# Performance work log

Measured on AMD Instinct MI355X. Metric: run time of the kernel, lower is better.

The kernel has to match this reference:

```python
import jax, jax.numpy as jnp
import numpy as np

B, T, D_IN, D_OUT, N_HEAD = 4, 2048, 1024, 1024, 16
HEAD_DIM = D_OUT // N_HEAD


def setup_inputs() -> dict:
    key = jax.random.key(0)
    ks = jax.random.split(key, 6)
    s_in = 1.0 / np.sqrt(D_IN)
    s_out = 1.0 / np.sqrt(D_OUT)
    return {
        "x": jax.random.normal(ks[0], (B, T, D_IN), dtype=jnp.float32),
        "Wq": jax.random.uniform(ks[1], (D_OUT, D_IN), jnp.float32, -s_in, s_in),
        "Wk": jax.random.uniform(ks[2], (D_OUT, D_IN), jnp.float32, -s_in, s_in),
        "Wv": jax.random.uniform(ks[3], (D_OUT, D_IN), jnp.float32, -s_in, s_in),
        "Wo": jax.random.uniform(ks[4], (D_OUT, D_OUT), jnp.float32, -s_out, s_out),
        "bo": jax.random.uniform(ks[5], (D_OUT,), jnp.float32, -s_out, s_out),
    }


def reference(x, Wq, Wk, Wv, Wo, bo):
    Bx, Tx, _ = x.shape
    # torch Linear: y = x @ W.T
    def heads(W):
        h = jnp.einsum("btc,dc->btd", x, W)
        return h.reshape(Bx, Tx, N_HEAD, HEAD_DIM).transpose(0, 2, 1, 3)  # [B,H,T,hd]
    q, k, v = heads(Wq), heads(Wk), heads(Wv)
    scores = jnp.einsum("bhqd,bhkd->bhqk", q, k)  # [B,H,T,T]
    causal = jnp.triu(jnp.ones((Tx, Tx), dtype=bool), k=1)
    scores = jnp.where(causal, -jnp.inf, scores)
    att = jax.nn.softmax(scores / np.sqrt(HEAD_DIM), axis=-1)
    ctx = jnp.einsum("bhqk,bhkd->bhqd", att, v)
    ctx = ctx.transpose(0, 2, 1, 3).reshape(Bx, Tx, D_OUT)
    return jnp.einsum("btd,od->bto", ctx, Wo) + bo
```

## Files before the change

### kernel.cpp

```cpp
#include <hip/hip_runtime.h>
#include <math.h>

typedef __attribute__((ext_vector_type(8))) short vbf8;
typedef __attribute__((ext_vector_type(4))) short vbf4;
typedef __attribute__((ext_vector_type(4))) float vf4;
typedef __attribute__((ext_vector_type(2))) unsigned int vu2;

__device__ __forceinline__ short f2bf(float f) {
  union { float f; unsigned int u; } v; v.f = f;
  unsigned int r = v.u + 0x7fffu + ((v.u >> 16) & 1u);
  return (short)(r >> 16);
}
__device__ __forceinline__ unsigned int cvtpk(float a, float b) {
  unsigned int r;
  asm("v_cvt_pk_bf16_f32 %0, %1, %2" : "=v"(r) : "v"(a), "v"(b));
  return r;
}
__device__ __forceinline__ float fexp2(float x) {
#if __has_builtin(__builtin_amdgcn_exp2f)
  return __builtin_amdgcn_exp2f(x);
#else
  return exp2f(x);
#endif
}

__device__ __forceinline__ void gload16(const void* g, void* l) {
  __builtin_amdgcn_global_load_lds(
      (const __attribute__((address_space(1))) unsigned int*)g,
      (__attribute__((address_space(3))) unsigned int*)l, 16, 0, 0);
}

__global__ __launch_bounds__(256) void cvt_kernel(const float* __restrict__ src,
                                                  short* __restrict__ dst, int n) {
  int i = (blockIdx.x * 256 + threadIdx.x) * 4;
  if (i >= n) return;
  float4 v = *(const float4*)(src + i);
  vu2 o;
  o.x = cvtpk(v.x, v.y);
  o.y = cvtpk(v.z, v.w);
  *(vu2*)(dst + i) = o;
}

__global__ __launch_bounds__(256) void cvtw_kernel(
    const float* __restrict__ Wq, const float* __restrict__ Wk,
    const float* __restrict__ Wv, short* __restrict__ wqkv) {
  const int bid = blockIdx.x;
  const int wsel = bid >> 10;
  const int off = ((bid & 1023) * 256 + threadIdx.x) * 4;
  const float* s = (wsel == 0) ? Wq : (wsel == 1) ? Wk : Wv;
  float4 v = *(const float4*)(s + off);
  vu2 o;
  o.x = cvtpk(v.x, v.y);
  o.y = cvtpk(v.z, v.w);
  *(vu2*)(wqkv + wsel * 1048576 + off) = o;
}

template <int EPI>
__global__ __launch_bounds__(256) void gemm_bt(
    const short* __restrict__ A, const short* __restrict__ Bw, int K,
    short* __restrict__ qb, short* __restrict__ kb, short* __restrict__ vtb,
    const float* __restrict__ bo, float* __restrict__ outp) {
  __shared__ __align__(16) short As[128 * 32];
  __shared__ __align__(16) short Bs[128 * 32];
  const int lane = threadIdx.x & 63;
  const int w = threadIdx.x >> 6;
  const int wr = w >> 1, wc = w & 1;

  const unsigned flat = blockIdx.y * gridDim.x + blockIdx.x;
  const unsigned cpx = (gridDim.x * gridDim.y) >> 3;
  const unsigned swz = (flat & 7) * cpx + (flat >> 3);
  const int m0 = (int)(swz / gridDim.x) * 128, n0 = (int)(swz % gridDim.x) * 128;

  const short* ga = A + (size_t)(m0 + w * 32 + (lane >> 2)) * K + (lane & 3) * 8;
  const short* gb = Bw + (size_t)(n0 + w * 32 + (lane >> 2)) * K + (lane & 3) * 8;
  short* lA = As + w * 1024;
  short* lB = Bs + w * 1024;

  vf4 acc[4][4];
#pragma unroll
  for (int i = 0; i < 4; ++i)
#pragma unroll
    for (int j = 0; j < 4; ++j) acc[i][j] = (vf4){0.f, 0.f, 0.f, 0.f};

  const int ar = wr * 64 + (lane & 15);
  const int br = wc * 64 + (lane & 15);
  const int kk = (lane >> 4) * 8;

  for (int k0 = 0; k0 < K; k0 += 32) {
    gload16(ga + k0, lA);
    gload16(ga + k0 + 16 * K, lA + 512);
    gload16(gb + k0, lB);
    gload16(gb + k0 + 16 * K, lB + 512);
    __syncthreads();
    vbf8 af[4], bfr[4];
#pragma unroll
    for (int mf = 0; mf < 4; ++mf) af[mf] = *(const vbf8*)(As + (ar + mf * 16) * 32 + kk);
#pragma unroll
    for (int nf = 0; nf < 4; ++nf) bfr[nf] = *(const vbf8*)(Bs + (br + nf * 16) * 32 + kk);
#pragma unroll
    for (int mf = 0; mf < 4; ++mf)
#pragma unroll
      for (int nf = 0; nf < 4; ++nf)
        acc[mf][nf] = __builtin_amdgcn_mfma_f32_16x16x32_bf16(af[mf], bfr[nf], acc[mf][nf], 0, 0, 0);
    __syncthreads();
  }

#pragma unroll
  for (int mf = 0; mf < 4; ++mf) {
    const int mbase = m0 + wr * 64 + mf * 16 + (lane >> 4) * 4;
#pragma unroll
    for (int nf = 0; nf < 4; ++nf) {
      vf4 v = acc[mf][nf];
      const int n = n0 + wc * 64 + nf * 16 + (lane & 15);
      if (EPI == 0) {
        const int region = n >> 10;
        const int nn = n & 1023;
        const int h = nn >> 6, d = nn & 63;
        if (region == 0) {
#pragma unroll
          for (int i = 0; i < 4; ++i) {
            const int m = mbase + i;
            const int b = m >> 11, t = m & 2047;
            qb[((size_t)(b * 16 + h) * 2048 + t) * 64 + d] = f2bf(v[i] * 0.1803368801111204f);
          }
        } else if (region == 1) {
#pragma unroll
          for (int i = 0; i < 4; ++i) {
            const int m = mbase + i;
            const int b = m >> 11, t = m & 2047;
            kb[((size_t)(b * 16 + h) * 2048 + t) * 64 + d] = f2bf(v[i]);
          }
        } else {
          const int b = mbase >> 11, t = mbase & 2047;
          vbf4 o;
          o.x = f2bf(v.x); o.y = f2bf(v.y); o.z = f2bf(v.z); o.w = f2bf(v.w);
          *(vbf4*)(vtb + ((size_t)(b * 16 + h) * 64 + d) * 2048 + t) = o;
        }
      } else {
        const float bias = bo[n];
#pragma unroll
        for (int i = 0; i < 4; ++i) {
          const int m = mbase + i;
          outp[(size_t)m * 1024 + n] = v[i] + bias;
        }
      }
    }
  }
}

__global__ __launch_bounds__(64) void attn_kernel(
    const short* __restrict__ Qh, const short* __restrict__ Kh,
    const short* __restrict__ Vt, short* __restrict__ ctx) {
  __shared__ __align__(16) short Ps[16 * 68];

  const int lane = threadIdx.x;
  const int l15 = lane & 15, g = lane >> 4;
  const int bid = blockIdx.x;
  const int x = bid & 7;
  const int kidx = bid >> 3;
  const int p_idx = kidx & 7;
  const int W = 31 - (kidx >> 3);
  const int pair = x + 8 * p_idx;
  const int b = pair >> 4, h = pair & 15;

  const size_t bhoff = (size_t)pair * 131072;
  const short* Qp = Qh + bhoff;
  const short* Kp = Kh + bhoff;
  const short* Vp = Vt + bhoff;
  const int wq0 = W * 64;

  vbf8 qfr[4][2];
#pragma unroll
  for (int qfi = 0; qfi < 4; ++qfi)
#pragma unroll
    for (int ks = 0; ks < 2; ++ks)
      qfr[qfi][ks] = *(const vbf8*)(Qp + (size_t)(wq0 + qfi * 16 + l15) * 64 +
                                    ks * 32 + g * 8);

  vf4 o2[4][4];
  float mrow[4], lrow[4];
#pragma unroll
  for (int qfi = 0; qfi < 4; ++qfi) {
#pragma unroll
    for (int df = 0; df < 4; ++df) o2[qfi][df] = (vf4){0.f, 0.f, 0.f, 0.f};
    mrow[qfi] = -1e30f; lrow[qfi] = 0.f;
  }

  const int nt = W + 1;

  vbf8 kA[4][2], kB[4][2];
  auto loadK = [&](int tt, vbf8 (&kd)[4][2]) {
    const int kb0 = tt * 64;
#pragma unroll
    for (int kf = 0; kf < 4; ++kf)
#pragma unroll
      for (int ks = 0; ks < 2; ++ks)
        kd[kf][ks] = *(const vbf8*)(Kp + (size_t)(kb0 + kf * 16 + l15) * 64 +
                                    ks * 32 + g * 8);
  };
  loadK(0, kA);

  auto tile = [&](int t, vbf8 (&kc)[4][2], vbf8 (&kn)[4][2]) {
    const int k0 = t * 64;

    vbf8 vb[2][4];
#pragma unroll
    for (int ks2 = 0; ks2 < 2; ++ks2)
#pragma unroll
      for (int df = 0; df < 4; ++df)
        vb[ks2][df] = *(const vbf8*)(Vp + (size_t)(df * 16 + l15) * 2048 +
                                     k0 + ks2 * 32 + g * 8);
    if (t + 1 < nt) loadK(t + 1, kn);

#pragma unroll
    for (int qfi = 0; qfi < 4; ++qfi) {
      const int q = wq0 + qfi * 16 + l15;
      const bool needmask = (k0 + 64 > wq0 + qfi * 16);

      vf4 s[4];
      __builtin_amdgcn_s_setprio(1);
#pragma unroll
      for (int kf = 0; kf < 4; ++kf) {
        s[kf] = (vf4){0.f, 0.f, 0.f, 0.f};
#pragma unroll
        for (int ks = 0; ks < 2; ++ks)
          s[kf] = __builtin_amdgcn_mfma_f32_16x16x32_bf16(kc[kf][ks], qfr[qfi][ks],
                                                          s[kf], 0, 0, 0);
      }
      __builtin_amdgcn_s_setprio(0);

      if (needmask) {
#pragma unroll
        for (int kf = 0; kf < 4; ++kf) {
          const int kbase = k0 + kf * 16 + g * 4;
#pragma unroll
          for (int i = 0; i < 4; ++i)
            if (kbase + i > q) s[kf][i] = -1e30f;
        }
      }
      float t0 = fmaxf(fmaxf(s[0][0], s[0][1]), fmaxf(s[0][2], s[0][3]));
      float t1 = fmaxf(fmaxf(s[1][0], s[1][1]), fmaxf(s[1][2], s[1][3]));
      float t2 = fmaxf(fmaxf(s[2][0], s[2][1]), fmaxf(s[2][2], s[2][3]));
      float t3 = fmaxf(fmaxf(s[3][0], s[3][1]), fmaxf(s[3][2], s[3][3]));
      const float mxl = fmaxf(fmaxf(t0, t1), fmaxf(t2, t3));

      float mn = mrow[qfi];
      if (!__all((int)(mxl - mn <= 8.f))) {
        float mx = fmaxf(mxl, __shfl_xor(mxl, 16));
        mx = fmaxf(mx, __shfl_xor(mx, 32));
        mn = fmaxf(mrow[qfi], mx);
        const float al = fexp2(mrow[qfi] - mn);
        mrow[qfi] = mn;
        lrow[qfi] *= al;
#pragma unroll
        for (int df = 0; df < 4; ++df)
#pragma unroll
          for (int i = 0; i < 4; ++i) o2[qfi][df][i] *= al;
      }

      float rs = 0.f;
#pragma unroll
      for (int kf = 0; kf < 4; ++kf)
#pragma unroll
        for (int i = 0; i < 4; ++i) {
          const float p = fexp2(s[kf][i] - mn);
          s[kf][i] = p;
          rs += p;
        }
      lrow[qfi] += rs;

#pragma unroll
      for (int kf = 0; kf < 4; ++kf) {
        vu2 pk;
        pk.x = cvtpk(s[kf][0], s[kf][1]);
        pk.y = cvtpk(s[kf][2], s[kf][3]);
        *(vu2*)(Ps + l15 * 68 + kf * 16 + g * 4) = pk;
      }

      vbf8 pb[2];
#pragma unroll
      for (int ks2 = 0; ks2 < 2; ++ks2)
        pb[ks2] = *(const vbf8*)(Ps + l15 * 68 + ks2 * 32 + g * 8);

      __builtin_amdgcn_s_setprio(1);
#pragma unroll
      for (int ks2 = 0; ks2 < 2; ++ks2)
#pragma unroll
        for (int df = 0; df < 4; ++df)
          o2[qfi][df] = __builtin_amdgcn_mfma_f32_16x16x32_bf16(vb[ks2][df], pb[ks2],
                                                                o2[qfi][df], 0, 0, 0);
      __builtin_amdgcn_s_setprio(0);
    }
  };

  for (int t = 0; t < nt; t += 2) {
    tile(t, kA, kB);
    if (t + 1 < nt) tile(t + 1, kB, kA);
  }

#pragma unroll
  for (int qfi = 0; qfi < 4; ++qfi) {
    float lsum = lrow[qfi];
    lsum += __shfl_xor(lsum, 16);
    lsum += __shfl_xor(lsum, 32);
    const float inv = 1.f / lsum;
    const int q = wq0 + qfi * 16 + l15;
    short* dst = ctx + (size_t)(b * 2048 + q) * 1024 + h * 64;
#pragma unroll
    for (int df = 0; df < 4; ++df) {
      vu2 o;
      o.x = cvtpk(o2[qfi][df][0] * inv, o2[qfi][df][1] * inv);
      o.y = cvtpk(o2[qfi][df][2] * inv, o2[qfi][df][3] * inv);
      *(vu2*)(dst + df * 16 + g * 4) = o;
    }
  }
}

extern "C" void kernel_launch(void* const* d_in, const int* in_sizes, int n_in,
                              void* d_out, int out_size, void* d_ws, size_t ws_size,
                              hipStream_t stream) {
  const float* x  = (const float*)d_in[0];
  const float* Wq = (const float*)d_in[1];
  const float* Wk = (const float*)d_in[2];
  const float* Wv = (const float*)d_in[3];
  const float* Wo = (const float*)d_in[4];
  const float* bo = (const float*)d_in[5];
  float* out = (float*)d_out;

  char* ws = (char*)d_ws;
  short* xb   = (short*)(ws);
  short* wqkv = (short*)(ws + 16777216);
  short* qb   = (short*)(ws + 23068672);
  short* kb   = (short*)(ws + 39845888);
  short* vtb  = (short*)(ws + 56623104);
  short* ctxb = xb;
  short* wob  = wqkv;

  cvt_kernel<<<8192, 256, 0, stream>>>(x, xb, 8388608);
  cvtw_kernel<<<3072, 256, 0, stream>>>(Wq, Wk, Wv, wqkv);
  gemm_bt<0><<<dim3(24, 64), 256, 0, stream>>>(xb, wqkv, 1024, qb, kb, vtb, nullptr, nullptr);
  cvt_kernel<<<1024, 256, 0, stream>>>(Wo, wob, 1048576);
  attn_kernel<<<2048, 64, 0, stream>>>(qb, kb, vtb, ctxb);
  gemm_bt<1><<<dim3(8, 64), 256, 0, stream>>>(ctxb, wob, 1024, nullptr, nullptr, nullptr, bo, out);
}
```

Before: 206.9 us.

## Replace QKV projection GEMM with 256x256-tile double-buffered kernel using direct global-to-LDS loads

The QKV projection GEMM now uses a new 512-thread kernel with 256x256 output tiles and a K-step of 64. It double-buffers LDS with gload16 direct global-to-shared loads, XOR-swizzles the LDS layout, and sets explicit waitcnt, barrier and priority scheduling. The goal is more data reuse per tile and hiding global load latency behind MFMA work. The cost is a large LDS footprint (128KB) and only 384 blocks, which may leave CUs idle and limit occupancy. The output projection keeps the old 128x128 kernel, now specialized without the template.

```diff
diff --git a/kernel.cpp b/kernel.cpp
--- a/kernel.cpp
+++ b/kernel.cpp
@@ -55,10 +55,125 @@
   *(vu2*)(wqkv + wsel * 1048576 + off) = o;
 }
 
-template <int EPI>
-__global__ __launch_bounds__(256) void gemm_bt(
+__global__ __launch_bounds__(512) void gemm256(
+    const short* __restrict__ A, const short* __restrict__ Bw,
+    short* __restrict__ qb, short* __restrict__ kb, short* __restrict__ vtb) {
+  __shared__ __align__(16) short As[2][16384];
+  __shared__ __align__(16) short Bs[2][16384];
+  const int tid = threadIdx.x;
+  const int lane = tid & 63;
+  const int w = tid >> 6;
+  const int wr = w >> 2, wc = w & 3;
+  const int l15 = lane & 15, g = lane >> 4;
+  const int K = 1024;
+
+  const unsigned flat = blockIdx.y * gridDim.x + blockIdx.x;
+  const unsigned cpx = (gridDim.x * gridDim.y) >> 3;
+  const unsigned swz = (flat & 7) * cpx + (flat >> 3);
+  const int m0 = (int)(swz / gridDim.x) * 256;
+  const int n0 = (int)(swz % gridDim.x) * 256;
+
+  const int srow = w * 32 + (lane >> 3);
+  const int scol = ((lane & 7) ^ (lane >> 3)) * 8;
+  const short* gA = A + (size_t)(m0 + srow) * K + scol;
+  const short* gB = Bw + (size_t)(n0 + srow) * K + scol;
+
+  vf4 acc[8][4];
+#pragma unroll
+  for (int i = 0; i < 8; ++i)
+#pragma unroll
+    for (int j = 0; j < 4; ++j) acc[i][j] = (vf4){0.f, 0.f, 0.f, 0.f};
+
+  auto stage2 = [&](int t, int bb, int q) {
+    const int koff = t * 64;
+    gload16(gA + (size_t)q * 8 * K + koff, &As[bb][(w * 32 + q * 8) * 64]);
+    gload16(gB + (size_t)q * 8 * K + koff, &Bs[bb][(w * 32 + q * 8) * 64]);
+  };
+
+#pragma unroll
+  for (int q = 0; q < 4; ++q) stage2(0, 0, q);
+
+  const int NT = 16;
+  for (int t = 0; t < NT; ++t) {
+    const int bb = t & 1;
+    vbf8 bfr[4][2];
+#pragma unroll
+    for (int q = 0; q < 4; ++q) {
+      if (t + 1 < NT) stage2(t + 1, bb ^ 1, q);
+      if (q == 0) {
+        if (t + 1 < NT) asm volatile("s_waitcnt vmcnt(2)" ::: "memory");
+        else            asm volatile("s_waitcnt vmcnt(0)" ::: "memory");
+        __builtin_amdgcn_s_barrier();
+#pragma unroll
+        for (int nf = 0; nf < 4; ++nf)
+#pragma unroll
+          for (int ks = 0; ks < 2; ++ks) {
+            const int r = wc * 64 + nf * 16 + l15;
+            const int c = (ks * 32 + g * 8) ^ ((r & 7) * 8);
+            bfr[nf][ks] = *(const vbf8*)(&Bs[bb][r * 64 + c]);
+          }
+      }
+      vbf8 afr[2][2];
+#pragma unroll
+      for (int i = 0; i < 2; ++i)
+#pragma unroll
+        for (int ks = 0; ks < 2; ++ks) {
+          const int r = wr * 128 + (q * 2 + i) * 16 + l15;
+          const int c = (ks * 32 + g * 8) ^ ((r & 7) * 8);
+          afr[i][ks] = *(const vbf8*)(&As[bb][r * 64 + c]);
+        }
+      asm volatile("s_waitcnt lgkmcnt(0)" ::: "memory");
+      __builtin_amdgcn_sched_barrier(0);
+      __builtin_amdgcn_s_setprio(1);
+#pragma unroll
+      for (int i = 0; i < 2; ++i)
+#pragma unroll
+        for (int nf = 0; nf < 4; ++nf)
+#pragma unroll
+          for (int ks = 0; ks < 2; ++ks)
+            acc[q * 2 + i][nf] = __builtin_amdgcn_mfma_f32_16x16x32_bf16(
+                afr[i][ks], bfr[nf][ks], acc[q * 2 + i][nf], 0, 0, 0);
+      __builtin_amdgcn_s_setprio(0);
+      if (q == 3) __builtin_amdgcn_s_barrier();
+    }
+  }
+
+#pragma unroll
+  for (int mf = 0; mf < 8; ++mf) {
+    const int mbase = m0 + wr * 128 + mf * 16 + g * 4;
+#pragma unroll
+    for (int nf = 0; nf < 4; ++nf) {
+      vf4 v = acc[mf][nf];
+      const int n = n0 + wc * 64 + nf * 16 + l15;
+      const int region = n >> 10;
+      const int nn = n & 1023;
+      const int h = nn >> 6, d = nn & 63;
+      if (region == 0) {
+#pragma unroll
+        for (int i = 0; i < 4; ++i) {
+          const int m = mbase + i;
+          const int b = m >> 11, tt = m & 2047;
+          qb[((size_t)(b * 16 + h) * 2048 + tt) * 64 + d] = f2bf(v[i] * 0.1803368801111204f);
+        }
+      } else if (region == 1) {
+#pragma unroll
+        for (int i = 0; i < 4; ++i) {
+          const int m = mbase + i;
+          const int b = m >> 11, tt = m & 2047;
+          kb[((size_t)(b * 16 + h) * 2048 + tt) * 64 + d] = f2bf(v[i]);
+        }
+      } else {
+        const int b = mbase >> 11, tt = mbase & 2047;
+        vbf4 o;
+        o.x = f2bf(v.x); o.y = f2bf(v.y); o.z = f2bf(v.z); o.w = f2bf(v.w);
+        *(vbf4*)(vtb + ((size_t)(b * 16 + h) * 64 + d) * 2048 + tt) = o;
+      }
+    }
+  }
+}
+
+__global__ __launch_bounds__(256) void gemm_bt1(
     const short* __restrict__ A, const short* __restrict__ Bw, int K,
-    short* __restrict__ qb, short* __restrict__ kb, short* __restrict__ vtb,
     const float* __restrict__ bo, float* __restrict__ outp) {
   __shared__ __align__(16) short As[128 * 32];
   __shared__ __align__(16) short Bs[128 * 32];
@@ -112,37 +227,11 @@
     for (int nf = 0; nf < 4; ++nf) {
       vf4 v = acc[mf][nf];
       const int n = n0 + wc * 64 + nf * 16 + (lane & 15);
-      if (EPI == 0) {
-        const int region = n >> 10;
-        const int nn = n & 1023;
-        const int h = nn >> 6, d = nn & 63;
-        if (region == 0) {
-#pragma unroll
-          for (int i = 0; i < 4; ++i) {
-            const int m = mbase + i;
-            const int b = m >> 11, t = m & 2047;
-            qb[((size_t)(b * 16 + h) * 2048 + t) * 64 + d] = f2bf(v[i] * 0.1803368801111204f);
-          }
-        } else if (region == 1) {
-#pragma unroll
-          for (int i = 0; i < 4; ++i) {
-            const int m = mbase + i;
-            const int b = m >> 11, t = m & 2047;
-            kb[((size_t)(b * 16 + h) * 2048 + t) * 64 + d] = f2bf(v[i]);
-          }
-        } else {
-          const int b = mbase >> 11, t = mbase & 2047;
-          vbf4 o;
-          o.x = f2bf(v.x); o.y = f2bf(v.y); o.z = f2bf(v.z); o.w = f2bf(v.w);
-          *(vbf4*)(vtb + ((size_t)(b * 16 + h) * 64 + d) * 2048 + t) = o;
-        }
-      } else {
-        const float bias = bo[n];
-#pragma unroll
-        for (int i = 0; i < 4; ++i) {
-          const int m = mbase + i;
-          outp[(size_t)m * 1024 + n] = v[i] + bias;
-        }
+      const float bias = bo[n];
+#pragma unroll
+      for (int i = 0; i < 4; ++i) {
+        const int m = mbase + i;
+        outp[(size_t)m * 1024 + n] = v[i] + bias;
       }
     }
   }
@@ -338,8 +427,8 @@
 
   cvt_kernel<<<8192, 256, 0, stream>>>(x, xb, 8388608);
   cvtw_kernel<<<3072, 256, 0, stream>>>(Wq, Wk, Wv, wqkv);
-  gemm_bt<0><<<dim3(24, 64), 256, 0, stream>>>(xb, wqkv, 1024, qb, kb, vtb, nullptr, nullptr);
+  gemm256<<<dim3(12, 32), 512, 0, stream>>>(xb, wqkv, qb, kb, vtb);
   cvt_kernel<<<1024, 256, 0, stream>>>(Wo, wob, 1048576);
   attn_kernel<<<2048, 64, 0, stream>>>(qb, kb, vtb, ctxb);
-  gemm_bt<1><<<dim3(8, 64), 256, 0, stream>>>(ctxb, wob, 1024, nullptr, nullptr, nullptr, bo, out);
-}
+  gemm_bt1<<<dim3(8, 64), 256, 0, stream>>>(ctxb, wob, 1024, bo, out);
+}
```

New measurement: 216.4 us. 4.6% more time.

## Share K/V tiles in LDS across two waves and pair causal strips

Applied to the files above, without the earlier changes.

The attention kernel now runs two waves per block that share swizzled, double-buffered K and V tiles staged into LDS via direct global-to-LDS loads, instead of each single-wave block loading K/V into registers. Each block processes two 128-row query strips, one long and one short (15-Sp and Sp), so every block gets an equal causal workload, and the grid shrinks from 2048 to 512 blocks. The goal is to halve global K/V traffic per query row and balance causal work across blocks. In exchange it adds block-wide barriers and vmcnt waits every tile and lowers the block count. The wave owning the lower rows also idles on the final diagonal tile.

```diff
diff --git a/kernel.cpp b/kernel.cpp
--- a/kernel.cpp
+++ b/kernel.cpp
@@ -148,18 +148,22 @@
   }
 }
 
-__global__ __launch_bounds__(64) void attn_kernel(
+__global__ __launch_bounds__(128) void attn_kernel(
     const short* __restrict__ Qh, const short* __restrict__ Kh,
     const short* __restrict__ Vt, short* __restrict__ ctx) {
-  __shared__ __align__(16) short Ps[16 * 68];
-
-  const int lane = threadIdx.x;
+  __shared__ __align__(16) short Ks[2][64 * 64];
+  __shared__ __align__(16) short Vs[2][64 * 64];
+  __shared__ __align__(16) short Ps[2][16 * 68];
+
+  const int tid = threadIdx.x;
+  const int lane = tid & 63;
+  const int w = tid >> 6;
   const int l15 = lane & 15, g = lane >> 4;
   const int bid = blockIdx.x;
   const int x = bid & 7;
   const int kidx = bid >> 3;
   const int p_idx = kidx & 7;
-  const int W = 31 - (kidx >> 3);
+  const int Sp = kidx >> 3;
   const int pair = x + 8 * p_idx;
   const int b = pair >> 4, h = pair & 15;
 
@@ -167,153 +171,164 @@
   const short* Qp = Qh + bhoff;
   const short* Kp = Kh + bhoff;
   const short* Vp = Vt + bhoff;
-  const int wq0 = W * 64;
-
-  vbf8 qfr[4][2];
-#pragma unroll
-  for (int qfi = 0; qfi < 4; ++qfi)
-#pragma unroll
-    for (int ks = 0; ks < 2; ++ks)
-      qfr[qfi][ks] = *(const vbf8*)(Qp + (size_t)(wq0 + qfi * 16 + l15) * 64 +
-                                    ks * 32 + g * 8);
-
-  vf4 o2[4][4];
-  float mrow[4], lrow[4];
-#pragma unroll
-  for (int qfi = 0; qfi < 4; ++qfi) {
-#pragma unroll
-    for (int df = 0; df < 4; ++df) o2[qfi][df] = (vf4){0.f, 0.f, 0.f, 0.f};
-    mrow[qfi] = -1e30f; lrow[qfi] = 0.f;
-  }
-
-  const int nt = W + 1;
-
-  vbf8 kA[4][2], kB[4][2];
-  auto loadK = [&](int tt, vbf8 (&kd)[4][2]) {
-    const int kb0 = tt * 64;
-#pragma unroll
-    for (int kf = 0; kf < 4; ++kf)
+  const int sr = lane >> 3;
+  const int scol = ((lane & 7) ^ sr) * 8;
+  short* Pw = Ps[w];
+
+  auto runStrip = [&](int S) {
+    const int wq0 = S * 128 + w * 64;
+    const int nt = 2 * S + 2;
+
+    vbf8 qfr[4][2];
+#pragma unroll
+    for (int qfi = 0; qfi < 4; ++qfi)
 #pragma unroll
       for (int ks = 0; ks < 2; ++ks)
-        kd[kf][ks] = *(const vbf8*)(Kp + (size_t)(kb0 + kf * 16 + l15) * 64 +
-                                    ks * 32 + g * 8);
-  };
-  loadK(0, kA);
-
-  auto tile = [&](int t, vbf8 (&kc)[4][2], vbf8 (&kn)[4][2]) {
-    const int k0 = t * 64;
-
-    vbf8 vb[2][4];
-#pragma unroll
-    for (int ks2 = 0; ks2 < 2; ++ks2)
-#pragma unroll
-      for (int df = 0; df < 4; ++df)
-        vb[ks2][df] = *(const vbf8*)(Vp + (size_t)(df * 16 + l15) * 2048 +
-                                     k0 + ks2 * 32 + g * 8);
-    if (t + 1 < nt) loadK(t + 1, kn);
-
+        qfr[qfi][ks] = *(const vbf8*)(Qp + (size_t)(wq0 + qfi * 16 + l15) * 64 +
+                                      ks * 32 + g * 8);
+
+    vf4 o2[4][4];
+    float mrow[4], lrow[4];
 #pragma unroll
     for (int qfi = 0; qfi < 4; ++qfi) {
-      const int q = wq0 + qfi * 16 + l15;
-      const bool needmask = (k0 + 64 > wq0 + qfi * 16);
-
-      vf4 s[4];
-      __builtin_amdgcn_s_setprio(1);
-#pragma unroll
-      for (int kf = 0; kf < 4; ++kf) {
-        s[kf] = (vf4){0.f, 0.f, 0.f, 0.f};
-#pragma unroll
-        for (int ks = 0; ks < 2; ++ks)
-          s[kf] = __builtin_amdgcn_mfma_f32_16x16x32_bf16(kc[kf][ks], qfr[qfi][ks],
-                                                          s[kf], 0, 0, 0);
-      }
-      __builtin_amdgcn_s_setprio(0);
-
-      if (needmask) {
-#pragma unroll
-        for (int kf = 0; kf < 4; ++kf) {
-          const int kbase = k0 + kf * 16 + g * 4;
-#pragma unroll
-          for (int i = 0; i < 4; ++i)
-            if (kbase + i > q) s[kf][i] = -1e30f;
+#pragma unroll
+      for (int df = 0; df < 4; ++df) o2[qfi][df] = (vf4){0.f, 0.f, 0.f, 0.f};
+      mrow[qfi] = -1e30f; lrow[qfi] = 0.f;
+    }
+
+    auto stage = [&](int tt, int bb) {
+      const int k0s = tt * 64;
+#pragma unroll
+      for (int j = 0; j < 4; ++j)
+        gload16(Kp + (size_t)(k0s + w * 32 + j * 8 + sr) * 64 + scol,
+                &Ks[bb][(w * 32 + j * 8) * 64]);
+#pragma unroll
+      for (int j = 0; j < 4; ++j)
+        gload16(Vp + (size_t)(w * 32 + j * 8 + sr) * 2048 + k0s + scol,
+                &Vs[bb][(w * 32 + j * 8) * 64]);
+    };
+
+    stage(0, 0);
+    asm volatile("s_waitcnt vmcnt(0)" ::: "memory");
+    __builtin_amdgcn_s_barrier();
+
+    for (int t = 0; t < nt; ++t) {
+      const int bb = t & 1;
+      if (t + 1 < nt) stage(t + 1, bb ^ 1);
+
+      if (t <= 2 * S + w) {
+        const int k0 = t * 64;
+#pragma unroll
+        for (int qfi = 0; qfi < 4; ++qfi) {
+          const int q = wq0 + qfi * 16 + l15;
+          const bool needmask = (k0 + 64 > wq0 + qfi * 16);
+
+          vf4 s[4];
+          __builtin_amdgcn_s_setprio(1);
+#pragma unroll
+          for (int kf = 0; kf < 4; ++kf) {
+            s[kf] = (vf4){0.f, 0.f, 0.f, 0.f};
+#pragma unroll
+            for (int ks = 0; ks < 2; ++ks) {
+              const vbf8 kfrag = *(const vbf8*)(&Ks[bb][(kf * 16 + l15) * 64 +
+                                                        ((ks * 4 + g) ^ (l15 & 7)) * 8]);
+              s[kf] = __builtin_amdgcn_mfma_f32_16x16x32_bf16(kfrag, qfr[qfi][ks],
+                                                              s[kf], 0, 0, 0);
+            }
+          }
+          __builtin_amdgcn_s_setprio(0);
+
+          if (needmask) {
+#pragma unroll
+            for (int kf = 0; kf < 4; ++kf) {
+              const int kbase = k0 + kf * 16 + g * 4;
+#pragma unroll
+              for (int i = 0; i < 4; ++i)
+                if (kbase + i > q) s[kf][i] = -1e30f;
+            }
+          }
+          float t0 = fmaxf(fmaxf(s[0][0], s[0][1]), fmaxf(s[0][2], s[0][3]));
+          float t1 = fmaxf(fmaxf(s[1][0], s[1][1]), fmaxf(s[1][2], s[1][3]));
+          float t2 = fmaxf(fmaxf(s[2][0], s[2][1]), fmaxf(s[2][2], s[2][3]));
+          float t3 = fmaxf(fmaxf(s[3][0], s[3][1]), fmaxf(s[3][2], s[3][3]));
+          const float mxl = fmaxf(fmaxf(t0, t1), fmaxf(t2, t3));
+
+          float mn = mrow[qfi];
+          if (!__all((int)(mxl - mn <= 8.f))) {
+            float mx = fmaxf(mxl, __shfl_xor(mxl, 16));
+            mx = fmaxf(mx, __shfl_xor(mx, 32));
+            mn = fmaxf(mrow[qfi], mx);
+            const float al = fexp2(mrow[qfi] - mn);
+            mrow[qfi] = mn;
+            lrow[qfi] *= al;
+#pragma unroll
+            for (int df = 0; df < 4; ++df)
+#pragma unroll
+              for (int i = 0; i < 4; ++i) o2[qfi][df][i] *= al;
+          }
+
+          float rs = 0.f;
+#pragma unroll
+          for (int kf = 0; kf < 4; ++kf)
+#pragma unroll
+            for (int i = 0; i < 4; ++i) {
+              const float p = fexp2(s[kf][i] - mn);
+              s[kf][i] = p;
+              rs += p;
+            }
+          lrow[qfi] += rs;
+
+#pragma unroll
+          for (int kf = 0; kf < 4; ++kf) {
+            vu2 pk;
+            pk.x = cvtpk(s[kf][0], s[kf][1]);
+            pk.y = cvtpk(s[kf][2], s[kf][3]);
+            *(vu2*)(Pw + l15 * 68 + kf * 16 + g * 4) = pk;
+          }
+
+          vbf8 pb[2];
+#pragma unroll
+          for (int ks2 = 0; ks2 < 2; ++ks2)
+            pb[ks2] = *(const vbf8*)(Pw + l15 * 68 + ks2 * 32 + g * 8);
+
+          __builtin_amdgcn_s_setprio(1);
+#pragma unroll
+          for (int ks2 = 0; ks2 < 2; ++ks2)
+#pragma unroll
+            for (int df = 0; df < 4; ++df) {
+              const vbf8 vfrag = *(const vbf8*)(&Vs[bb][(df * 16 + l15) * 64 +
+                                                        ((ks2 * 4 + g) ^ (l15 & 7)) * 8]);
+              o2[qfi][df] = __builtin_amdgcn_mfma_f32_16x16x32_bf16(vfrag, pb[ks2],
+                                                                    o2[qfi][df], 0, 0, 0);
+            }
+          __builtin_amdgcn_s_setprio(0);
         }
       }
-      float t0 = fmaxf(fmaxf(s[0][0], s[0][1]), fmaxf(s[0][2], s[0][3]));
-      float t1 = fmaxf(fmaxf(s[1][0], s[1][1]), fmaxf(s[1][2], s[1][3]));
-      float t2 = fmaxf(fmaxf(s[2][0], s[2][1]), fmaxf(s[2][2], s[2][3]));
-      float t3 = fmaxf(fmaxf(s[3][0], s[3][1]), fmaxf(s[3][2], s[3][3]));
-      const float mxl = fmaxf(fmaxf(t0, t1), fmaxf(t2, t3));
-
-      float mn = mrow[qfi];
-      if (!__all((int)(mxl - mn <= 8.f))) {
-        float mx = fmaxf(mxl, __shfl_xor(mxl, 16));
-        mx = fmaxf(mx, __shfl_xor(mx, 32));
-        mn = fmaxf(mrow[qfi], mx);
-        const float al = fexp2(mrow[qfi] - mn);
-        mrow[qfi] = mn;
-        lrow[qfi] *= al;
-#pragma unroll
-        for (int df = 0; df < 4; ++df)
-#pragma unroll
-          for (int i = 0; i < 4; ++i) o2[qfi][df][i] *= al;
+
+      asm volatile("s_waitcnt vmcnt(0)" ::: "memory");
+      __builtin_amdgcn_s_barrier();
+    }
+
+#pragma unroll
+    for (int qfi = 0; qfi < 4; ++qfi) {
+      float lsum = lrow[qfi];
+      lsum += __shfl_xor(lsum, 16);
+      lsum += __shfl_xor(lsum, 32);
+      const float inv = 1.f / lsum;
+      const int q = wq0 + qfi * 16 + l15;
+      short* dst = ctx + (size_t)(b * 2048 + q) * 1024 + h * 64;
+#pragma unroll
+      for (int df = 0; df < 4; ++df) {
+        vu2 o;
+        o.x = cvtpk(o2[qfi][df][0] * inv, o2[qfi][df][1] * inv);
+        o.y = cvtpk(o2[qfi][df][2] * inv, o2[qfi][df][3] * inv);
+        *(vu2*)(dst + df * 16 + g * 4) = o;
       }
-
-      float rs = 0.f;
-#pragma unroll
-      for (int kf = 0; kf < 4; ++kf)
-#pragma unroll
-        for (int i = 0; i < 4; ++i) {
-          const float p = fexp2(s[kf][i] - mn);
-          s[kf][i] = p;
-          rs += p;
-        }
-      lrow[qfi] += rs;
-
-#pragma unroll
-      for (int kf = 0; kf < 4; ++kf) {
-        vu2 pk;
-        pk.x = cvtpk(s[kf][0], s[kf][1]);
-        pk.y = cvtpk(s[kf][2], s[kf][3]);
-        *(vu2*)(Ps + l15 * 68 + kf * 16 + g * 4) = pk;
-      }
-
-      vbf8 pb[2];
-#pragma unroll
-      for (int ks2 = 0; ks2 < 2; ++ks2)
-        pb[ks2] = *(const vbf8*)(Ps + l15 * 68 + ks2 * 32 + g * 8);
-
-      __builtin_amdgcn_s_setprio(1);
-#pragma unroll
-      for (int ks2 = 0; ks2 < 2; ++ks2)
-#pragma unroll
-        for (int df = 0; df < 4; ++df)
-          o2[qfi][df] = __builtin_amdgcn_mfma_f32_16x16x32_bf16(vb[ks2][df], pb[ks2],
-                                                                o2[qfi][df], 0, 0, 0);
-      __builtin_amdgcn_s_setprio(0);
     }
   };
 
-  for (int t = 0; t < nt; t += 2) {
-    tile(t, kA, kB);
-    if (t + 1 < nt) tile(t + 1, kB, kA);
-  }
-
-#pragma unroll
-  for (int qfi = 0; qfi < 4; ++qfi) {
-    float lsum = lrow[qfi];
-    lsum += __shfl_xor(lsum, 16);
-    lsum += __shfl_xor(lsum, 32);
-    const float inv = 1.f / lsum;
-    const int q = wq0 + qfi * 16 + l15;
-    short* dst = ctx + (size_t)(b * 2048 + q) * 1024 + h * 64;
-#pragma unroll
-    for (int df = 0; df < 4; ++df) {
-      vu2 o;
-      o.x = cvtpk(o2[qfi][df][0] * inv, o2[qfi][df][1] * inv);
-      o.y = cvtpk(o2[qfi][df][2] * inv, o2[qfi][df][3] * inv);
-      *(vu2*)(dst + df * 16 + g * 4) = o;
-    }
-  }
+  runStrip(15 - Sp);
+  runStrip(Sp);
 }
 
 extern "C" void kernel_launch(void* const* d_in, const int* in_sizes, int n_in,
@@ -340,6 +355,6 @@
   cvtw_kernel<<<3072, 256, 0, stream>>>(Wq, Wk, Wv, wqkv);
   gemm_bt<0><<<dim3(24, 64), 256, 0, stream>>>(xb, wqkv, 1024, qb, kb, vtb, nullptr, nullptr);
   cvt_kernel<<<1024, 256, 0, stream>>>(Wo, wob, 1048576);
-  attn_kernel<<<2048, 64, 0, stream>>>(qb, kb, vtb, ctxb);
+  attn_kernel<<<512, 128, 0, stream>>>(qb, kb, vtb, ctxb);
   gemm_bt<1><<<dim3(8, 64), 256, 0, stream>>>(ctxb, wob, 1024, nullptr, nullptr, nullptr, bo, out);
 }
```

Result: slower. 249.3 us (+20.5%).
